# Kernel optimization log

Measured on AMD Instinct MI355X. Metric: run time of the kernel, lower is better.

## Reference

```python
import jax, jax.numpy as jnp
from jax import lax
import numpy as np


def setup_inputs() -> dict:
    key = jax.random.key(0)
    B, N, K_ORDERS = 8, 16384, 4
    k1, k2 = jax.random.split(key)
    coord = jax.random.normal(k1, (B * N, 3), dtype=jnp.float32)
    serialized_code = jax.random.randint(k2, (K_ORDERS, B * N), 0, 1 << 30)
    return {
        "coord": coord,
        "serialized_code": serialized_code,
        "batch_size": 8,
        "num_group": 1024,
        "group_size": 32,
    }


def _fps(pts, G):
    """Farthest point sampling on pts [N,3]; starts at index 0 (pointops convention)."""
    N = pts.shape[0]

    def step(carry, _):
        dist, last = carry
        d = jnp.sum((pts - pts[last]) ** 2, axis=-1)  # [N]
        dist = jnp.minimum(dist, d)
        nxt = jnp.argmax(dist).astype(jnp.int32)
        return (dist, nxt), nxt

    init = (jnp.full((N,), jnp.inf, pts.dtype), jnp.int32(0))
    _, rest = lax.scan(step, init, None, length=G - 1)
    return jnp.concatenate([jnp.zeros((1,), jnp.int32), rest])  # [G]


def reference(coord, serialized_code, batch_size, num_group, group_size):
    B, G, S = batch_size, num_group, group_size
    N = coord.shape[0] // B
    pts = coord.reshape(B, N, 3)

    # --- FPS per cloud (offset-batched in the original) ---
    loc_idx = jax.vmap(lambda p: _fps(p, G))(pts)  # [B, G] local indices
    s_idx = (loc_idx + (jnp.arange(B, dtype=jnp.int32) * N)[:, None]).reshape(-1)  # [B*G] global
    s_xyz = coord[s_idx]  # [B*G, 3]

    # --- KNN per cloud: S nearest points to each sampled center ---
    centers = s_xyz.reshape(B, G, 3)

    def knn_one(p, c):  # p [N,3], c [G,3]
        # squared distances via gemm to avoid [G,N,3] intermediate
        d2 = (jnp.sum(c * c, -1)[:, None] + jnp.sum(p * p, -1)[None, :]
              - 2.0 * c @ p.T)  # [G, N]
        _, idx = lax.top_k(-d2, S)  # ascending distance, self first
        return idx

    nloc = jax.vmap(knn_one)(pts, centers)  # [B, G, S]
    s_n_idx = (nloc + (jnp.arange(B) * N)[:, None, None]).reshape(B * G, S)

    # relative coords, drop the self point (column 0)
    s_n = coord[s_n_idx] - s_xyz[:, None, :]  # [B*G, S, 3]
    s_n = s_n[:, 1:, :]  # [B*G, S-1, 3]

    # --- serialization order over sampled points + inverse permutation ---
    code_sel = serialized_code[:, s_idx]  # [K, B*G]
    s_order = jnp.argsort(code_sel, axis=1)  # [K, B*G]
    M = s_order.shape[1]
    src = jnp.broadcast_to(jnp.arange(M, dtype=s_order.dtype), s_order.shape)
    rows = jnp.arange(s_order.shape[0])[:, None]
    s_inverse = jnp.zeros_like(s_order).at[rows, s_order].set(src)

    return s_idx, s_n, s_xyz, s_order, s_inverse
```

## Files before the change

kernel.cpp:

```cpp
#include <hip/hip_runtime.h>
#include <hip/hip_bf16.h>
#include <stdint.h>

#define BB 8
#define NN 16384
#define GG 1024
#define SS 32
#define BN (BB*NN)

#define OFF_SIDX 0
#define OFF_SN   8192
#define OFF_SXYZ 770048
#define OFF_ORD  794624
#define OFF_INV  827392

#define WS_SIDX 0
#define WS_KNN  32768

typedef float v2f __attribute__((ext_vector_type(2)));
typedef unsigned long long u64x2 __attribute__((ext_vector_type(2)));

static __device__ __forceinline__ v2f vmin2(v2f a, v2f b) {
    v2f r; r.x = fminf(a.x, b.x); r.y = fminf(a.y, b.y); return r;
}
static __device__ __forceinline__ v2f vmax2(v2f a, v2f b) {
    v2f r; r.x = fmaxf(a.x, b.x); r.y = fmaxf(a.y, b.y); return r;
}

template<int CTRL, int RM, int BM>
static __device__ __forceinline__ unsigned dpp_umax(unsigned v) {
    unsigned o = (unsigned)__builtin_amdgcn_update_dpp((int)v, (int)v, CTRL, RM, BM, false);
    return o > v ? o : v;
}

template<int CTRL, int RM, int BM>
static __device__ __forceinline__ uint64_t dpp_umin64(uint64_t v) {
    unsigned lo = (unsigned)v, hi = (unsigned)(v >> 32);
    unsigned olo = (unsigned)__builtin_amdgcn_update_dpp((int)lo, (int)lo, CTRL, RM, BM, false);
    unsigned ohi = (unsigned)__builtin_amdgcn_update_dpp((int)hi, (int)hi, CTRL, RM, BM, false);
    uint64_t o = ((uint64_t)ohi << 32) | olo;
    return o < v ? o : v;
}

static __device__ __forceinline__ uint64_t wave_umin64(uint64_t v) {
    v = dpp_umin64<0x111, 0xf, 0xf>(v);
    v = dpp_umin64<0x112, 0xf, 0xf>(v);
    v = dpp_umin64<0x114, 0xf, 0xf>(v);
    v = dpp_umin64<0x118, 0xf, 0xf>(v);
    v = dpp_umin64<0x142, 0xa, 0xf>(v);
    v = dpp_umin64<0x143, 0xc, 0xf>(v);
    return v;
}

static __device__ __forceinline__ uint64_t rdlane64(uint64_t v, int sl) {
    unsigned lo = (unsigned)__builtin_amdgcn_readlane((int)(unsigned)v, sl);
    unsigned hi = (unsigned)__builtin_amdgcn_readlane((int)(unsigned)(v >> 32), sl);
    return ((uint64_t)hi << 32) | lo;
}

static __device__ __forceinline__ unsigned mono(float f) {
    unsigned u = __float_as_uint(f);
    return u ^ (unsigned)((((int)u) >> 31) | (int)0x80000000u);
}

__global__ __launch_bounds__(512, 2)
void fps_kernel(const float* __restrict__ coord,
                int* __restrict__ ws_sidx,
                float* __restrict__ out) {
#pragma clang fp contract(off)
    const int b = blockIdx.x;
    const int t = threadIdx.x;
    const int base = b * NN;
    const int wave = t >> 6, lane = t & 63;

    const float q0x = coord[3*base], q0y = coord[3*base+1], q0z = coord[3*base+2];

    const float* my = coord + 3*(base + t*32);

    v2f px[16], py[16], pz[16];
#pragma unroll
    for (int j = 0; j < 16; j++) {
        px[j] = (v2f){my[6*j  ], my[6*j+3]};
        py[j] = (v2f){my[6*j+1], my[6*j+4]};
        pz[j] = (v2f){my[6*j+2], my[6*j+5]};
        asm volatile("" : "+v"(px[j]));
        asm volatile("" : "+v"(py[j]));
        asm volatile("" : "+v"(pz[j]));
    }

    v2f dist[16];
#pragma unroll
    for (int j = 0; j < 16; j++) {
        v2f dx = px[j] - (v2f){q0x,q0x};
        v2f dy = py[j] - (v2f){q0y,q0y};
        v2f dz = pz[j] - (v2f){q0z,q0z};
        dist[j] = (dx*dx + dy*dy) + dz*dz;
    }

    __shared__ unsigned wv[8];
    __shared__ unsigned win[2];

    if (t == 0) {
        ws_sidx[b*GG] = base;
        out[OFF_SIDX + b*GG] = (float)base;
        win[0] = 0xffffffffu; win[1] = 0xffffffffu;
    }
    __syncthreads();

    for (int g = 1; g < GG; g++) {
        const int s = g & 1;
        v2f m0 = vmax2(vmax2(dist[0], dist[1]),  vmax2(dist[2], dist[3]));
        v2f m1 = vmax2(vmax2(dist[4], dist[5]),  vmax2(dist[6], dist[7]));
        v2f m2 = vmax2(vmax2(dist[8], dist[9]),  vmax2(dist[10], dist[11]));
        v2f m3 = vmax2(vmax2(dist[12], dist[13]),vmax2(dist[14], dist[15]));
        v2f m07 = vmax2(vmax2(m0, m1), vmax2(m2, m3));
        float bvf = fmaxf(m07.x, m07.y);
        unsigned lb = __float_as_uint(bvf);
        unsigned r = lb;
        r = dpp_umax<0x111, 0xf, 0xf>(r);
        r = dpp_umax<0x112, 0xf, 0xf>(r);
        r = dpp_umax<0x114, 0xf, 0xf>(r);
        r = dpp_umax<0x118, 0xf, 0xf>(r);
        r = dpp_umax<0x142, 0xa, 0xf>(r);
        r = dpp_umax<0x143, 0xc, 0xf>(r);
        unsigned wmax = (unsigned)__builtin_amdgcn_readlane((int)r, 63);
        if (lane == 0) wv[wave] = wmax;
        __syncthreads();
        if (t == 0) win[1 - s] = 0xffffffffu;
        unsigned x = wv[lane & 7];
        x = dpp_umax<0x111, 0xf, 0xf>(x);
        x = dpp_umax<0x112, 0xf, 0xf>(x);
        x = dpp_umax<0x114, 0xf, 0xf>(x);
        unsigned bmax = (unsigned)__builtin_amdgcn_readlane((int)x, 7);
        if (lb == bmax) {
            int e = 31;
#pragma unroll
            for (int jj = 31; jj >= 0; jj--) {
                float v = (jj & 1) ? dist[jj >> 1].y : dist[jj >> 1].x;
                if (__float_as_uint(v) == bmax) e = jj;
            }
            atomicMin(&win[s], (unsigned)(t*32 + e));
        }
        __syncthreads();
        unsigned pw = win[s];
        int sp = __builtin_amdgcn_readfirstlane((int)pw);
        if (t == 0) {
            ws_sidx[b*GG + g] = base + sp;
            out[OFF_SIDX + b*GG + g] = (float)(base + sp);
        }
        float qx = coord[3*(base+sp)];
        float qy = coord[3*(base+sp)+1];
        float qz = coord[3*(base+sp)+2];
        v2f qvx = (v2f){qx,qx}, qvy = (v2f){qy,qy}, qvz = (v2f){qz,qz};
#pragma unroll
        for (int j = 0; j < 16; j++) {
            v2f dx = px[j] - qvx, dy = py[j] - qvy, dz = pz[j] - qvz;
            v2f d  = (dx*dx + dy*dy) + dz*dz;
            dist[j] = vmin2(dist[j], d);
        }
    }
}

__global__ __launch_bounds__(64) void knn_kernel(const float* __restrict__ coord,
                                                 const int* __restrict__ ws_sidx,
                                                 int* __restrict__ ws_knn) {
#pragma clang fp contract(off)
    const int c = blockIdx.x;
    const int l = threadIdx.x;
    const int b = c >> 10;
    const int base = b * NN;
    const int sg = ws_sidx[c];
    const float cx = coord[3*sg], cy = coord[3*sg+1], cz = coord[3*sg+2];
    const float cc = (cx*cx + cy*cy) + cz*cz;

    uint64_t k1 = ~0ull, k2 = ~0ull;
#pragma unroll 4
    for (int j = 0; j < 256; j++) {
        int p = l + (j << 6);
        float x = coord[3*(base+p)], y = coord[3*(base+p)+1], z = coord[3*(base+p)+2];
        float pp  = (x*x + y*y) + z*z;
        float dot = (cx*x + cy*y) + cz*z;
        float d2  = (cc + pp) - 2.0f*dot;
        uint64_t key = (((uint64_t)mono(d2)) << 14) | (unsigned)p;
        if (key < k1)      { k2 = k1; k1 = key; }
        else if (key < k2) { k2 = key; }
    }

    uint64_t m0 = 0, m1 = 0, m2 = 0, m3 = 0;
    uint64_t cur = k1, nxt = k2;
    bool have_nxt = true;
    int res_p = 0;
    for (int k = 0; k < SS; k++) {
        uint64_t wmin = wave_umin64(cur);
        uint64_t bkey = rdlane64(wmin, 63);
        const int bp = (int)(bkey & 16383u);
        const int w  = bp & 63;
        const int e  = bp >> 6;
        if (l == k) res_p = bp;
        bool need_rescan = false;
        if (l == w) {
            uint64_t bit = 1ull << (e & 63);
            int word = e >> 6;
            if      (word == 0) m0 |= bit;
            else if (word == 1) m1 |= bit;
            else if (word == 2) m2 |= bit;
            else                m3 |= bit;
            if (have_nxt) { cur = nxt; have_nxt = false; }
            else need_rescan = true;
        }
        if (__ballot(need_rescan)) {
            uint64_t w0 = rdlane64(m0, w), w1 = rdlane64(m1, w),
                     w2 = rdlane64(m2, w), w3 = rdlane64(m3, w);
            uint64_t best = ~0ull;
#pragma unroll
            for (int m = 0; m < 4; m++) {
                int e2 = l + (m << 6);
                uint64_t mw = (m == 0) ? w0 : ((m == 1) ? w1 : ((m == 2) ? w2 : w3));
                int p2 = w + (e2 << 6);
                float x = coord[3*(base+p2)], y = coord[3*(base+p2)+1], z = coord[3*(base+p2)+2];
                float pp  = (x*x + y*y) + z*z;
                float dot = (cx*x + cy*y) + cz*z;
                float d2  = (cc + pp) - 2.0f*dot;
                uint64_t key = (((uint64_t)mono(d2)) << 14) | (unsigned)p2;
                bool cons = (mw >> l) & 1ull;
                if (!cons && key < best) best = key;
            }
            best = wave_umin64(best);
            uint64_t rk = rdlane64(best, 63);
            if (l == w) cur = rk;
        }
    }
    if (l < SS) ws_knn[c * SS + l] = res_p;
}

__global__ void sxyz_kernel(const float* __restrict__ coord,
                            const int* __restrict__ ws_sidx,
                            float* __restrict__ out) {
    int t = blockIdx.x * blockDim.x + threadIdx.x;
    if (t < 8192*3) {
        int i = t / 3, cmp = t - 3*i;
        out[OFF_SXYZ + t] = coord[3*ws_sidx[i] + cmp];
    }
}

__global__ void sn_kernel(const float* __restrict__ coord,
                          const int* __restrict__ ws_sidx,
                          const int* __restrict__ ws_knn,
                          float* __restrict__ out) {
#pragma clang fp contract(off)
    int t = blockIdx.x * blockDim.x + threadIdx.x;
    if (t < 8192*31*3) {
        int cmp = t % 3; int rem = t / 3;
        int j = rem % 31; int i = rem / 31;
        int b = i >> 10;
        int nb = ws_knn[i*SS + j + 1];
        int gidx = b*NN + nb;
        float v = coord[3*gidx + cmp] - coord[3*ws_sidx[i] + cmp];
        out[OFF_SN + t] = v;
    }
}

__global__ __launch_bounds__(1024) void sort_kernel(const int* __restrict__ ser,
                                                    const int* __restrict__ ws_sidx,
                                                    float* __restrict__ out) {
    __shared__ __align__(16) uint64_t keys[8192];
    const int r = blockIdx.x, t = threadIdx.x;
    uint64_t e[8];
#pragma unroll
    for (int m = 0; m < 8; m++) {
        int i = t*8 + m;
        uint32_t code = (uint32_t)ser[r * BN + ws_sidx[i]];
        e[m] = ((uint64_t)code << 13) | (uint32_t)i;
    }
#define CE(a, b, up) { uint64_t xa = e[a], xb = e[b]; \
                       if ((xa > xb) == (up)) { e[a] = xb; e[b] = xa; } }
    CE(0,1,true) CE(2,3,false) CE(4,5,true) CE(6,7,false)
    CE(0,2,true) CE(1,3,true) CE(4,6,false) CE(5,7,false)
    CE(0,1,true) CE(2,3,true) CE(4,5,false) CE(6,7,false)
    {
        bool up = ((t & 1) == 0);
        CE(0,4,up) CE(1,5,up) CE(2,6,up) CE(3,7,up)
        CE(0,2,up) CE(1,3,up) CE(4,6,up) CE(5,7,up)
        CE(0,1,up) CE(2,3,up) CE(4,5,up) CE(6,7,up)
    }
    u64x2* kp = (u64x2*)keys;
    for (int k2 = 16; k2 <= 8192; k2 <<= 1) {
        const bool up = ((t & (k2 >> 3)) == 0);
        for (int j = k2 >> 1; j >= 8; j >>= 1) {
#pragma unroll
            for (int q = 0; q < 4; q++)
                kp[t*4 + q] = (u64x2){e[2*q], e[2*q+1]};
            __syncthreads();
            const int pt = t ^ (j >> 3);
            uint64_t pb[8];
#pragma unroll
            for (int q = 0; q < 4; q++) {
                u64x2 v = kp[pt*4 + q];
                pb[2*q] = v.x; pb[2*q+1] = v.y;
            }
            const bool lower = ((t & (j >> 3)) == 0);
            const bool keepmin = (lower == up);
#pragma unroll
            for (int m = 0; m < 8; m++) {
                uint64_t a = e[m], bq = pb[m];
                uint64_t mn = a < bq ? a : bq;
                uint64_t mx = a < bq ? bq : a;
                e[m] = keepmin ? mn : mx;
            }
            __syncthreads();
        }
        CE(0,4,up) CE(1,5,up) CE(2,6,up) CE(3,7,up)
        CE(0,2,up) CE(1,3,up) CE(4,6,up) CE(5,7,up)
        CE(0,1,up) CE(2,3,up) CE(4,5,up) CE(6,7,up)
    }
#undef CE
#pragma unroll
    for (int m = 0; m < 8; m++) {
        int k = t*8 + m;
        uint64_t key = e[m];
        int i = (int)(key & 8191u);
        out[OFF_ORD + r*8192 + k] = (float)i;
        out[OFF_INV + r*8192 + i] = (float)k;
    }
}

extern "C" void kernel_launch(void* const* d_in, const int* in_sizes, int n_in,
                              void* d_out, int out_size, void* d_ws, size_t ws_size,
                              hipStream_t stream) {
    const float* coord = (const float*)d_in[0];
    const int* ser = (const int*)d_in[1];
    float* out = (float*)d_out;
    char* ws = (char*)d_ws;
    int* ws_sidx = (int*)(ws + WS_SIDX);
    int* ws_knn  = (int*)(ws + WS_KNN);

    hipLaunchKernelGGL(fps_kernel,  dim3(BB),   dim3(512),  0, stream, coord, ws_sidx, out);
    hipLaunchKernelGGL(knn_kernel,  dim3(8192), dim3(64),   0, stream, coord, ws_sidx, ws_knn);
    hipLaunchKernelGGL(sxyz_kernel, dim3(96),   dim3(256),  0, stream, coord, ws_sidx, out);
    hipLaunchKernelGGL(sn_kernel,   dim3(2976), dim3(256),  0, stream, coord, ws_sidx, ws_knn, out);
    hipLaunchKernelGGL(sort_kernel, dim3(4),    dim3(1024), 0, stream, ser, ws_sidx, out);
}
```

Before: 1.916 ms.

## Stage FPS x/y coordinates in LDS with strided point layout

Moves the per-thread x and y point coordinates of the FPS kernel from registers into LDS. Only z and the running distances stay in VGPRs. Points are reassigned with a stride of 512 threads so the initial global loads coalesce, and the winner index encoding is changed to match. Launch bounds drop to one block per CU to allow the larger LDS footprint. The aim is to cut register pressure, at the cost of extra LDS reads in every serial FPS iteration.

```diff
diff --git a/kernel.cpp b/kernel.cpp
--- a/kernel.cpp
+++ b/kernel.cpp
@@ -63,7 +63,7 @@
     return u ^ (unsigned)((((int)u) >> 31) | (int)0x80000000u);
 }
 
-__global__ __launch_bounds__(512, 2)
+__global__ __launch_bounds__(512, 1)
 void fps_kernel(const float* __restrict__ coord,
                 int* __restrict__ ws_sidx,
                 float* __restrict__ out) {
@@ -73,32 +73,30 @@
     const int base = b * NN;
     const int wave = t >> 6, lane = t & 63;
 
-    const float q0x = coord[3*base], q0y = coord[3*base+1], q0z = coord[3*base+2];
-
-    const float* my = coord + 3*(base + t*32);
-
-    v2f px[16], py[16], pz[16];
-#pragma unroll
-    for (int j = 0; j < 16; j++) {
-        px[j] = (v2f){my[6*j  ], my[6*j+3]};
-        py[j] = (v2f){my[6*j+1], my[6*j+4]};
-        pz[j] = (v2f){my[6*j+2], my[6*j+5]};
-        asm volatile("" : "+v"(px[j]));
-        asm volatile("" : "+v"(py[j]));
-        asm volatile("" : "+v"(pz[j]));
-    }
-
-    v2f dist[16];
-#pragma unroll
-    for (int j = 0; j < 16; j++) {
-        v2f dx = px[j] - (v2f){q0x,q0x};
-        v2f dy = py[j] - (v2f){q0y,q0y};
-        v2f dz = pz[j] - (v2f){q0z,q0z};
-        dist[j] = (dx*dx + dy*dy) + dz*dz;
-    }
-
+    __shared__ __align__(16) v2f lds_xp[8192];
+    __shared__ __align__(16) v2f lds_yp[8192];
     __shared__ unsigned wv[8];
     __shared__ unsigned win[2];
+
+    const float q0x = coord[3*base], q0y = coord[3*base+1], q0z = coord[3*base+2];
+
+    v2f pz[16], dist[16];
+#pragma unroll
+    for (int m = 0; m < 16; m++) {
+        const int p0 = t + (m << 10);
+        const int p1 = p0 + 512;
+        const float x0 = coord[3*(base+p0)], y0 = coord[3*(base+p0)+1], z0 = coord[3*(base+p0)+2];
+        const float x1 = coord[3*(base+p1)], y1 = coord[3*(base+p1)+1], z1 = coord[3*(base+p1)+2];
+        lds_xp[(m<<9)+t] = (v2f){x0, x1};
+        lds_yp[(m<<9)+t] = (v2f){y0, y1};
+        pz[m] = (v2f){z0, z1};
+        v2f dx = (v2f){x0,x1} - (v2f){q0x,q0x};
+        v2f dy = (v2f){y0,y1} - (v2f){q0y,q0y};
+        v2f dz = pz[m] - (v2f){q0z,q0z};
+        dist[m] = (dx*dx + dy*dy) + dz*dz;
+    }
+#pragma unroll
+    for (int m = 0; m < 16; m++) asm volatile("" : "+v"(pz[m]));
 
     if (t == 0) {
         ws_sidx[b*GG] = base;
@@ -139,7 +137,7 @@
                 float v = (jj & 1) ? dist[jj >> 1].y : dist[jj >> 1].x;
                 if (__float_as_uint(v) == bmax) e = jj;
             }
-            atomicMin(&win[s], (unsigned)(t*32 + e));
+            atomicMin(&win[s], (unsigned)(t + (e << 9)));
         }
         __syncthreads();
         unsigned pw = win[s];
@@ -153,10 +151,12 @@
         float qz = coord[3*(base+sp)+2];
         v2f qvx = (v2f){qx,qx}, qvy = (v2f){qy,qy}, qvz = (v2f){qz,qz};
 #pragma unroll
-        for (int j = 0; j < 16; j++) {
-            v2f dx = px[j] - qvx, dy = py[j] - qvy, dz = pz[j] - qvz;
+        for (int m = 0; m < 16; m++) {
+            v2f px = lds_xp[(m<<9)+t];
+            v2f py = lds_yp[(m<<9)+t];
+            v2f dx = px - qvx, dy = py - qvy, dz = pz[m] - qvz;
             v2f d  = (dx*dx + dy*dy) + dz*dz;
-            dist[j] = vmin2(dist[j], d);
+            dist[m] = vmin2(dist[m], d);
         }
     }
 }
```

Result: slower. 1.996 ms (+4.2%).

## Split each cloud's farthest point sampling across four blocks with global-atomic mailboxes

Applied to the files above, without the earlier changes.

The FPS kernel now launches four blocks per cloud, so 32 blocks in total, and each block holds a quarter of the points. That leaves 8 points per thread instead of 32. Every iteration, each block publishes its packed (max distance, inverted index) candidate to a double-buffered global mailbox and bumps a per-cloud counter. All threads then spin until the four blocks of that cloud have arrived and pick the global winner. This cuts per-iteration ALU and register work and spreads FPS over more CUs, but each of the 1023 serial iterations now pays a device-scope atomic round trip. That may cross XCDs, and all threads poll the counter.

```diff
diff --git a/kernel.cpp b/kernel.cpp
--- a/kernel.cpp
+++ b/kernel.cpp
@@ -63,23 +63,31 @@
     return u ^ (unsigned)((((int)u) >> 31) | (int)0x80000000u);
 }
 
-__global__ __launch_bounds__(512, 2)
+__global__ __launch_bounds__(512, 1)
 void fps_kernel(const float* __restrict__ coord,
                 int* __restrict__ ws_sidx,
+                unsigned* __restrict__ cnt_arr,
+                unsigned long long* __restrict__ mail,
                 float* __restrict__ out) {
 #pragma clang fp contract(off)
-    const int b = blockIdx.x;
-    const int t = threadIdx.x;
+    const int bk = blockIdx.x;
+    const int b  = bk & 7;
+    const int k  = bk >> 3;
+    const int t  = threadIdx.x;
     const int base = b * NN;
+    const int so   = k << 12;
     const int wave = t >> 6, lane = t & 63;
 
+    __shared__ unsigned wv[8];
+    __shared__ unsigned win[2];
+
     const float q0x = coord[3*base], q0y = coord[3*base+1], q0z = coord[3*base+2];
 
-    const float* my = coord + 3*(base + t*32);
-
-    v2f px[16], py[16], pz[16];
-#pragma unroll
-    for (int j = 0; j < 16; j++) {
+    const float* my = coord + 3*(base + so + t*8);
+
+    v2f px[4], py[4], pz[4];
+#pragma unroll
+    for (int j = 0; j < 4; j++) {
         px[j] = (v2f){my[6*j  ], my[6*j+3]};
         py[j] = (v2f){my[6*j+1], my[6*j+4]};
         pz[j] = (v2f){my[6*j+2], my[6*j+5]};
@@ -88,33 +96,30 @@
         asm volatile("" : "+v"(pz[j]));
     }
 
-    v2f dist[16];
-#pragma unroll
-    for (int j = 0; j < 16; j++) {
+    v2f dist[4];
+#pragma unroll
+    for (int j = 0; j < 4; j++) {
         v2f dx = px[j] - (v2f){q0x,q0x};
         v2f dy = py[j] - (v2f){q0y,q0y};
         v2f dz = pz[j] - (v2f){q0z,q0z};
         dist[j] = (dx*dx + dy*dy) + dz*dz;
     }
 
-    __shared__ unsigned wv[8];
-    __shared__ unsigned win[2];
-
     if (t == 0) {
-        ws_sidx[b*GG] = base;
-        out[OFF_SIDX + b*GG] = (float)base;
+        if (k == 0) {
+            ws_sidx[b*GG] = base;
+            out[OFF_SIDX + b*GG] = (float)base;
+        }
         win[0] = 0xffffffffu; win[1] = 0xffffffffu;
     }
     __syncthreads();
 
     for (int g = 1; g < GG; g++) {
         const int s = g & 1;
-        v2f m0 = vmax2(vmax2(dist[0], dist[1]),  vmax2(dist[2], dist[3]));
-        v2f m1 = vmax2(vmax2(dist[4], dist[5]),  vmax2(dist[6], dist[7]));
-        v2f m2 = vmax2(vmax2(dist[8], dist[9]),  vmax2(dist[10], dist[11]));
-        v2f m3 = vmax2(vmax2(dist[12], dist[13]),vmax2(dist[14], dist[15]));
-        v2f m07 = vmax2(vmax2(m0, m1), vmax2(m2, m3));
-        float bvf = fmaxf(m07.x, m07.y);
+        v2f m01 = vmax2(dist[0], dist[1]);
+        v2f m23 = vmax2(dist[2], dist[3]);
+        v2f m03 = vmax2(m01, m23);
+        float bvf = fmaxf(m03.x, m03.y);
         unsigned lb = __float_as_uint(bvf);
         unsigned r = lb;
         r = dpp_umax<0x111, 0xf, 0xf>(r);
@@ -133,18 +138,38 @@
         x = dpp_umax<0x114, 0xf, 0xf>(x);
         unsigned bmax = (unsigned)__builtin_amdgcn_readlane((int)x, 7);
         if (lb == bmax) {
-            int e = 31;
-#pragma unroll
-            for (int jj = 31; jj >= 0; jj--) {
+            int e = 7;
+#pragma unroll
+            for (int jj = 7; jj >= 0; jj--) {
                 float v = (jj & 1) ? dist[jj >> 1].y : dist[jj >> 1].x;
                 if (__float_as_uint(v) == bmax) e = jj;
             }
-            atomicMin(&win[s], (unsigned)(t*32 + e));
+            atomicMin(&win[s], (unsigned)(t*8 + e));
         }
         __syncthreads();
-        unsigned pw = win[s];
-        int sp = __builtin_amdgcn_readfirstlane((int)pw);
+        const unsigned pw = win[s];
+        const unsigned w_loc = (unsigned)so + pw;
+        const unsigned long long pack =
+            (((unsigned long long)bmax) << 32) | (unsigned long long)(16383u - w_loc);
         if (t == 0) {
+            __hip_atomic_store(&mail[b*8 + s*4 + k], pack,
+                               __ATOMIC_RELAXED, __HIP_MEMORY_SCOPE_AGENT);
+            __hip_atomic_fetch_add(&cnt_arr[b*16], 1u,
+                                   __ATOMIC_RELEASE, __HIP_MEMORY_SCOPE_AGENT);
+        }
+        const unsigned target = 4u * (unsigned)g;
+        while (__hip_atomic_load(&cnt_arr[b*16],
+                                 __ATOMIC_ACQUIRE, __HIP_MEMORY_SCOPE_AGENT) < target) { }
+        unsigned long long p0 = __hip_atomic_load(&mail[b*8 + s*4 + 0], __ATOMIC_RELAXED, __HIP_MEMORY_SCOPE_AGENT);
+        unsigned long long p1 = __hip_atomic_load(&mail[b*8 + s*4 + 1], __ATOMIC_RELAXED, __HIP_MEMORY_SCOPE_AGENT);
+        unsigned long long p2 = __hip_atomic_load(&mail[b*8 + s*4 + 2], __ATOMIC_RELAXED, __HIP_MEMORY_SCOPE_AGENT);
+        unsigned long long p3 = __hip_atomic_load(&mail[b*8 + s*4 + 3], __ATOMIC_RELAXED, __HIP_MEMORY_SCOPE_AGENT);
+        unsigned long long b01 = p0 > p1 ? p0 : p1;
+        unsigned long long b23 = p2 > p3 ? p2 : p3;
+        unsigned long long best = b01 > b23 ? b01 : b23;
+        int sp = (int)(16383u - (unsigned)(best & 0xFFFFu));
+        sp = __builtin_amdgcn_readfirstlane(sp);
+        if (k == 0 && t == 0) {
             ws_sidx[b*GG + g] = base + sp;
             out[OFF_SIDX + b*GG + g] = (float)(base + sp);
         }
@@ -153,7 +178,7 @@
         float qz = coord[3*(base+sp)+2];
         v2f qvx = (v2f){qx,qx}, qvy = (v2f){qy,qy}, qvz = (v2f){qz,qz};
 #pragma unroll
-        for (int j = 0; j < 16; j++) {
+        for (int j = 0; j < 4; j++) {
             v2f dx = px[j] - qvx, dy = py[j] - qvy, dz = pz[j] - qvz;
             v2f d  = (dx*dx + dy*dy) + dz*dz;
             dist[j] = vmin2(dist[j], d);
@@ -333,8 +358,12 @@
     char* ws = (char*)d_ws;
     int* ws_sidx = (int*)(ws + WS_SIDX);
     int* ws_knn  = (int*)(ws + WS_KNN);
-
-    hipLaunchKernelGGL(fps_kernel,  dim3(BB),   dim3(512),  0, stream, coord, ws_sidx, out);
+    unsigned* cnt_arr = (unsigned*)(ws + WS_KNN);
+    unsigned long long* mail = (unsigned long long*)(ws + WS_KNN + 512);
+
+    hipMemsetAsync(ws + WS_KNN, 0, 512, stream);
+
+    hipLaunchKernelGGL(fps_kernel,  dim3(32),   dim3(512),  0, stream, coord, ws_sidx, cnt_arr, mail, out);
     hipLaunchKernelGGL(knn_kernel,  dim3(8192), dim3(64),   0, stream, coord, ws_sidx, ws_knn);
     hipLaunchKernelGGL(sxyz_kernel, dim3(96),   dim3(256),  0, stream, coord, ws_sidx, out);
     hipLaunchKernelGGL(sn_kernel,   dim3(2976), dim3(256),  0, stream, coord, ws_sidx, ws_knn, out);
```

Result: slower. 6.650 ms (+247.1%).
